# Kernel optimization log

Measured on AMD Instinct MI355X. Metric: run time of the kernel, lower is better.

## Reference

```python
import jax, jax.numpy as jnp
import numpy as np

DIM = 256
HEADS = 4
DIM_HEAD = 32
HIDDEN = HEADS * DIM_HEAD  # 128
SCALE = DIM_HEAD ** -0.5
EPS = 1e-5


def setup_inputs() -> dict:
    key = jax.random.key(0)
    ks = jax.random.split(key, 6)
    B, H, W = 32, 64, 64
    x = jax.random.normal(ks[0], (B, DIM, H, W), dtype=jnp.float32)
    w_qkv = jax.random.normal(ks[1], (3 * HIDDEN, DIM), dtype=jnp.float32) * (DIM ** -0.5)
    w_out = jax.random.normal(ks[2], (DIM, HIDDEN), dtype=jnp.float32) * (HIDDEN ** -0.5)
    b_out = jnp.zeros((DIM,), dtype=jnp.float32)
    g = jnp.ones((DIM,), dtype=jnp.float32)
    b = jnp.zeros((DIM,), dtype=jnp.float32)
    return {"x": x, "w_qkv": w_qkv, "w_out": w_out, "b_out": b_out, "g": g, "b": b}


def reference(x, w_qkv, w_out, b_out, g, b):
    B, C, H, W = x.shape
    n = H * W
    # 1x1 conv qkv projection (no bias)
    qkv = jnp.einsum('oc,bchw->bohw', w_qkv, x)  # [B, 3*HIDDEN, H, W]
    qkv = qkv.reshape(B, 3, HEADS, DIM_HEAD, n)  # [B, 3, h, d, n]
    q, k, v = qkv[:, 0], qkv[:, 1], qkv[:, 2]
    q = jax.nn.softmax(q, axis=-2) * SCALE       # softmax over head dim d
    k = jax.nn.softmax(k, axis=-1)               # softmax over tokens n
    context = jnp.einsum('bhdn,bhen->bhde', k, v)
    out = jnp.einsum('bhde,bhdn->bhen', context, q)  # [B, h, e, n]
    out = out.reshape(B, HIDDEN, H, W)
    # 1x1 conv output projection with bias
    out = jnp.einsum('oc,bchw->bohw', w_out, out) + b_out[None, :, None, None]
    # LayerNorm over channel dim (biased variance)
    mean = jnp.mean(out, axis=1, keepdims=True)
    var = jnp.var(out, axis=1, keepdims=True)
    out = (out - mean) / jnp.sqrt(var + EPS) * g[None, :, None, None] + b[None, :, None, None]
    return out
```

## Files before the change

### kernel.cpp

```cpp
#include <hip/hip_runtime.h>
#include <math.h>

#define NPIX 4096
#define BATCH 32
#define CDIM 256
#define SCALE_F 0.17677669529663687f
#define EPS_F 1e-5f

typedef _Float16 f16;
typedef _Float16 f16x8 __attribute__((ext_vector_type(8)));
typedef _Float16 f16x4 __attribute__((ext_vector_type(4)));
typedef float    f32x4 __attribute__((ext_vector_type(4)));

static __device__ __forceinline__ f32x4 mfma16(f16x8 a, f16x8 b, f32x4 c) {
    return __builtin_amdgcn_mfma_f32_16x16x32_f16(a, b, c, 0, 0, 0);
}

__global__ __launch_bounds__(256)
void wconv(const float* __restrict__ w, f16* __restrict__ wh)
{
    int i = blockIdx.x * 256 + threadIdx.x;
    float4 v = ((const float4*)w)[i];
    f16x4 o = {(f16)v.x, (f16)v.y, (f16)v.z, (f16)v.w};
    ((f16x4*)wh)[i] = o;
}

__global__ __launch_bounds__(256)
void qkv_fused(const f16* __restrict__ wh, const float* __restrict__ x,
               f16* __restrict__ qhatT, float* __restrict__ ctx,
               float* __restrict__ ksum)
{
    __shared__ __align__(16) f16 As[384 * 32];
    __shared__ __align__(16) f16 Bs[64 * 32];
    __shared__ __align__(16) f16 ek_s[128 * 64];
    __shared__ __align__(16) f16 v_s[128 * 64];

    const int b = blockIdx.y;
    const int t = threadIdx.x;
    const int lane = t & 63, w = t >> 6;
    const int lane15 = lane & 15, lg = lane >> 4;
    const int grow = w * 96;

    const float* xb = x + (size_t)b * 256 * NPIX;
    f16* qT = qhatT + (size_t)b * NPIX * 128;

    const int bn = t & 63;
    const int bc = t >> 6;
    const int bsw = bn * 32 + ((bc ^ ((bn >> 1) & 3)) << 3);

    f32x4 ctxacc[2][2];
    const f32x4 z4 = {0.f, 0.f, 0.f, 0.f};
    ctxacc[0][0] = z4; ctxacc[0][1] = z4; ctxacc[1][0] = z4; ctxacc[1][1] = z4;

    for (int tile = 0; tile < 4; tile++) {
        const int n0 = blockIdx.x * 256 + tile * 64;
        f32x4 acc[6][4];
        #pragma unroll
        for (int i = 0; i < 6; i++)
            #pragma unroll
            for (int j = 0; j < 4; j++) acc[i][j] = z4;

        float v8[8];
        #pragma unroll
        for (int m = 0; m < 8; m++)
            v8[m] = xb[(size_t)(bc * 8 + m) * NPIX + n0 + bn];

        for (int ks = 0; ks < 8; ks++) {
            const int k0 = ks * 32;
            #pragma unroll
            for (int it = 0; it < 6; it++) {
                int c = t + it * 256;
                int row = c >> 2, ch = c & 3;
                *(f16x8*)&As[row * 32 + ((ch ^ ((row >> 1) & 3)) << 3)] =
                    *(const f16x8*)&wh[(size_t)row * 256 + k0 + ch * 8];
            }
            f16x8 bv;
            #pragma unroll
            for (int m = 0; m < 8; m++) bv[m] = (f16)v8[m];
            *(f16x8*)&Bs[bsw] = bv;
            __syncthreads();
            if (ks < 7) {
                #pragma unroll
                for (int m = 0; m < 8; m++)
                    v8[m] = xb[(size_t)(k0 + 32 + bc * 8 + m) * NPIX + n0 + bn];
            }
            f16x8 bf[4];
            #pragma unroll
            for (int j = 0; j < 4; j++) {
                int rr = j * 16 + lane15;
                bf[j] = *(const f16x8*)&Bs[rr * 32 + ((lg ^ ((rr >> 1) & 3)) << 3)];
            }
            #pragma unroll
            for (int i = 0; i < 6; i++) {
                int rr = grow + i * 16 + lane15;
                f16x8 af = *(const f16x8*)&As[rr * 32 + ((lg ^ ((rr >> 1) & 3)) << 3)];
                #pragma unroll
                for (int j = 0; j < 4; j++)
                    acc[i][j] = mfma16(af, bf[j], acc[i][j]);
            }
            __syncthreads();
        }

        #pragma unroll
        for (int i = 0; i < 6; i++) {
            const int rbase = grow + i * 16;
            if (rbase < 128) {
                if ((rbase & 31) == 0) {
                    #pragma unroll
                    for (int j = 0; j < 4; j++) {
                        float e0[2][4]; float s = 0.f;
                        #pragma unroll
                        for (int ii = 0; ii < 2; ii++)
                            #pragma unroll
                            for (int r = 0; r < 4; r++) {
                                float ev = __expf(acc[i + ii][j][r]);
                                e0[ii][r] = ev; s += ev;
                            }
                        s += __shfl_xor(s, 16); s += __shfl_xor(s, 32);
                        float inv = SCALE_F / s;
                        int n = n0 + j * 16 + lane15;
                        #pragma unroll
                        for (int ii = 0; ii < 2; ii++) {
                            int d0 = rbase + ii * 16 + lg * 4;
                            f16x4 pk;
                            #pragma unroll
                            for (int r = 0; r < 4; r++) pk[r] = (f16)(e0[ii][r] * inv);
                            *(f16x4*)(qT + (size_t)n * 128 + d0) = pk;
                        }
                    }
                }
            } else if (rbase < 256) {
                const int kb = rbase - 128;
                #pragma unroll
                for (int r = 0; r < 4; r++) {
                    int row = kb + lg * 4 + r;
                    float p = 0.f;
                    #pragma unroll
                    for (int j = 0; j < 4; j++) {
                        float ev = __expf(acc[i][j][r]);
                        p += ev;
                        int col = j * 16 + lane15;
                        ek_s[row * 64 + ((((col >> 3) ^ (row & 7)) << 3) | (col & 7))] =
                            (f16)ev;
                    }
                    p += __shfl_xor(p, 1); p += __shfl_xor(p, 2);
                    p += __shfl_xor(p, 4); p += __shfl_xor(p, 8);
                    if (lane15 == 0) atomicAdd(&ksum[b * 128 + row], p);
                }
            } else {
                const int vb = rbase - 256;
                #pragma unroll
                for (int r = 0; r < 4; r++) {
                    int row = vb + lg * 4 + r;
                    #pragma unroll
                    for (int j = 0; j < 4; j++) {
                        int col = j * 16 + lane15;
                        v_s[row * 64 + ((((col >> 3) ^ (row & 7)) << 3) | (col & 7))] =
                            (f16)acc[i][j][r];
                    }
                }
            }
        }
        __syncthreads();
        #pragma unroll
        for (int ks2 = 0; ks2 < 2; ks2++) {
            f16x8 a2[2], b2[2];
            #pragma unroll
            for (int i2 = 0; i2 < 2; i2++) {
                int row = w * 32 + i2 * 16 + lane15;
                int off = row * 64 + (((ks2 * 4 + lg) ^ (row & 7)) << 3);
                a2[i2] = *(const f16x8*)&ek_s[off];
                b2[i2] = *(const f16x8*)&v_s[off];
            }
            #pragma unroll
            for (int i2 = 0; i2 < 2; i2++)
                #pragma unroll
                for (int j2 = 0; j2 < 2; j2++)
                    ctxacc[i2][j2] = mfma16(a2[i2], b2[j2], ctxacc[i2][j2]);
        }
    }

    float* cg = ctx + ((size_t)b * 4 + w) * 1024;
    #pragma unroll
    for (int i2 = 0; i2 < 2; i2++)
        #pragma unroll
        for (int j2 = 0; j2 < 2; j2++)
            #pragma unroll
            for (int r = 0; r < 4; r++)
                atomicAdd(&cg[(i2 * 16 + lg * 4 + r) * 32 + j2 * 16 + lane15],
                          ctxacc[i2][j2][r]);
}

__global__ __launch_bounds__(256)
void weff_kernel(const float* __restrict__ wout, const float* __restrict__ ctx,
                 const float* __restrict__ ksum, f16* __restrict__ weff)
{
    const int bh = blockIdx.x;
    const int b = bh >> 2, h = bh & 3;
    __shared__ float cs[1024];
    __shared__ float inv_s[32];
    const int t = threadIdx.x;
    for (int i = t; i < 1024; i += 256) cs[i] = ctx[(size_t)bh * 1024 + i];
    if (t < 32) inv_s[t] = 1.f / ksum[b * 128 + h * 32 + t];
    __syncthreads();
    float acc[32] = {};
    const float* wrow = wout + (size_t)t * 128 + h * 32;
    for (int e = 0; e < 32; e++) {
        float wv = wrow[e];
        #pragma unroll
        for (int d = 0; d < 32; d++) acc[d] += wv * cs[d * 32 + e];
    }
    f16* wo = weff + ((size_t)b * 256 + t) * 128 + h * 32;
    #pragma unroll
    for (int d = 0; d < 32; d++) wo[d] = (f16)(acc[d] * inv_s[d]);
}

__global__ __launch_bounds__(256)
void out_mfma_ln(const f16* __restrict__ weff, const f16* __restrict__ qhatT,
                 const float* __restrict__ bias, const float* __restrict__ g,
                 const float* __restrict__ bb, float* __restrict__ out)
{
    __shared__ __align__(16) f16 As2[256 * 32];
    __shared__ __align__(16) f16 Bs2[128 * 32];
    __shared__ float pb[256], pg[256], pbb[256];
    __shared__ float lds_s[4][128], lds_s2[4][128];
    const int b = blockIdx.y;
    const int tileN = blockIdx.x * 128;
    const int t = threadIdx.x;
    const int lane = t & 63, w = t >> 6;
    const int lane15 = lane & 15, lg = lane >> 4;
    pb[t] = bias[t]; pg[t] = g[t]; pbb[t] = bb[t];
    const f16* Aw = weff + (size_t)b * 256 * 128;
    const f16* Bw = qhatT + (size_t)b * NPIX * 128;
    f32x4 acc[4][8];
    const f32x4 z4 = {0.f, 0.f, 0.f, 0.f};
    #pragma unroll
    for (int i = 0; i < 4; i++)
        #pragma unroll
        for (int j = 0; j < 8; j++) acc[i][j] = z4;

    for (int k0 = 0; k0 < 128; k0 += 32) {
        #pragma unroll
        for (int it = 0; it < 4; it++) {
            int c = t + it * 256;
            int row = c >> 2, koff = (c & 3) * 8;
            *(f16x8*)&As2[row * 32 + koff] = *(const f16x8*)&Aw[(size_t)row * 128 + k0 + koff];
        }
        #pragma unroll
        for (int it = 0; it < 2; it++) {
            int c = t + it * 256;
            int row = c >> 2, koff = (c & 3) * 8;
            *(f16x8*)&Bs2[row * 32 + koff] =
                *(const f16x8*)&Bw[(size_t)(tileN + row) * 128 + k0 + koff];
        }
        __syncthreads();
        f16x8 af[4], bf[8];
        #pragma unroll
        for (int i = 0; i < 4; i++)
            af[i] = *(const f16x8*)&As2[(w * 64 + i * 16 + lane15) * 32 + lg * 8];
        #pragma unroll
        for (int j = 0; j < 8; j++)
            bf[j] = *(const f16x8*)&Bs2[(j * 16 + lane15) * 32 + lg * 8];
        #pragma unroll
        for (int i = 0; i < 4; i++)
            #pragma unroll
            for (int j = 0; j < 8; j++)
                acc[i][j] = mfma16(af[i], bf[j], acc[i][j]);
        __syncthreads();
    }
    #pragma unroll
    for (int i = 0; i < 4; i++)
        #pragma unroll
        for (int r = 0; r < 4; r++) {
            float bo = pb[w * 64 + i * 16 + lg * 4 + r];
            #pragma unroll
            for (int j = 0; j < 8; j++) acc[i][j][r] += bo;
        }
    #pragma unroll
    for (int j = 0; j < 8; j++) {
        float s = 0.f, s2 = 0.f;
        #pragma unroll
        for (int i = 0; i < 4; i++)
            #pragma unroll
            for (int r = 0; r < 4; r++) { float v = acc[i][j][r]; s += v; s2 += v * v; }
        s += __shfl_xor(s, 16);  s += __shfl_xor(s, 32);
        s2 += __shfl_xor(s2, 16); s2 += __shfl_xor(s2, 32);
        if (lg == 0) { lds_s[w][j * 16 + lane15] = s; lds_s2[w][j * 16 + lane15] = s2; }
    }
    __syncthreads();
    float mean[8], rstd[8];
    #pragma unroll
    for (int j = 0; j < 8; j++) {
        int col = j * 16 + lane15;
        float S = lds_s[0][col] + lds_s[1][col] + lds_s[2][col] + lds_s[3][col];
        float S2 = lds_s2[0][col] + lds_s2[1][col] + lds_s2[2][col] + lds_s2[3][col];
        float mn = S * (1.f / 256.f);
        mean[j] = mn;
        rstd[j] = rsqrtf(S2 * (1.f / 256.f) - mn * mn + EPS_F);
    }
    float* ob = out + (size_t)b * CDIM * NPIX;
    #pragma unroll
    for (int i = 0; i < 4; i++)
        #pragma unroll
        for (int r = 0; r < 4; r++) {
            int row = w * 64 + i * 16 + lg * 4 + r;
            float gm = pg[row], bt = pbb[row];
            #pragma unroll
            for (int j = 0; j < 8; j++)
                ob[(size_t)row * NPIX + tileN + j * 16 + lane15] =
                    (acc[i][j][r] - mean[j]) * rstd[j] * gm + bt;
        }
}

extern "C" void kernel_launch(void* const* d_in, const int* in_sizes, int n_in,
                              void* d_out, int out_size, void* d_ws, size_t ws_size,
                              hipStream_t stream)
{
    const float* x     = (const float*)d_in[0];
    const float* w_qkv = (const float*)d_in[1];
    const float* w_out = (const float*)d_in[2];
    const float* b_out = (const float*)d_in[3];
    const float* g     = (const float*)d_in[4];
    const float* bvec  = (const float*)d_in[5];
    float* out = (float*)d_out;

    char* wsb = (char*)d_ws;
    f16*   qhatT = (f16*)wsb;
    float* ctx   = (float*)(wsb + 33554432);
    float* ksum  = (float*)(wsb + 34078720);
    f16*   weff  = (f16*)(wsb + 34095104);
    f16*   wh    = (f16*)(wsb + 36192256);

    hipMemsetAsync(ctx, 0, 540672, stream);
    wconv<<<96, 256, 0, stream>>>(w_qkv, wh);
    qkv_fused<<<dim3(16, BATCH), 256, 0, stream>>>(wh, x, qhatT, ctx, ksum);
    weff_kernel<<<128, 256, 0, stream>>>(w_out, ctx, ksum, weff);
    out_mfma_ln<<<dim3(32, BATCH), 256, 0, stream>>>(weff, qhatT, b_out, g, bvec, out);
}
```

Baseline: 349.3 us.

## Load QKV weight fragments directly from global into registers with double-buffered B tile

Removes the shared-memory staging of the 384x32 weight tile. Each lane now loads its MFMA A fragments straight from global (L2-resident) memory into registers, and they are prefetched one k-step ahead. The x tile uses two shared buffers, which cuts one barrier per k-step and overlaps the next loads with the MFMAs. This frees LDS and barrier overhead, at the cost of more VGPRs and uncoalesced global loads of the weights.

Result: slower. 416.6 us (+19.3%).

```diff
diff --git a/kernel.cpp b/kernel.cpp
--- a/kernel.cpp
+++ b/kernel.cpp
@@ -30,8 +30,7 @@
                f16* __restrict__ qhatT, float* __restrict__ ctx,
                float* __restrict__ ksum)
 {
-    __shared__ __align__(16) f16 As[384 * 32];
-    __shared__ __align__(16) f16 Bs[64 * 32];
+    __shared__ __align__(16) f16 Bs[2][64 * 32];
     __shared__ __align__(16) f16 ek_s[128 * 64];
     __shared__ __align__(16) f16 v_s[128 * 64];
 
@@ -48,10 +47,23 @@
     const int bc = t >> 6;
     const int bsw = bn * 32 + ((bc ^ ((bn >> 1) & 3)) << 3);
 
+    const f16* Ab = wh + (size_t)(grow + lane15) * 256 + lg * 8;
+
     f32x4 ctxacc[2][2];
     const f32x4 z4 = {0.f, 0.f, 0.f, 0.f};
     ctxacc[0][0] = z4; ctxacc[0][1] = z4; ctxacc[1][0] = z4; ctxacc[1][1] = z4;
 
+    f16x8 af[6], af2[6];
+    float v8[8];
+    {
+        const int n00 = blockIdx.x * 256;
+        #pragma unroll
+        for (int i = 0; i < 6; i++) af[i] = *(const f16x8*)&Ab[i * 4096];
+        #pragma unroll
+        for (int m2 = 0; m2 < 8; m2++)
+            v8[m2] = xb[(size_t)(bc * 8 + m2) * NPIX + n00 + bn];
+    }
+
     for (int tile = 0; tile < 4; tile++) {
         const int n0 = blockIdx.x * 256 + tile * 64;
         f32x4 acc[6][4];
@@ -60,45 +72,75 @@
             #pragma unroll
             for (int j = 0; j < 4; j++) acc[i][j] = z4;
 
-        float v8[8];
-        #pragma unroll
-        for (int m = 0; m < 8; m++)
-            v8[m] = xb[(size_t)(bc * 8 + m) * NPIX + n0 + bn];
-
-        for (int ks = 0; ks < 8; ks++) {
-            const int k0 = ks * 32;
-            #pragma unroll
-            for (int it = 0; it < 6; it++) {
-                int c = t + it * 256;
-                int row = c >> 2, ch = c & 3;
-                *(f16x8*)&As[row * 32 + ((ch ^ ((row >> 1) & 3)) << 3)] =
-                    *(const f16x8*)&wh[(size_t)row * 256 + k0 + ch * 8];
-            }
-            f16x8 bv;
-            #pragma unroll
-            for (int m = 0; m < 8; m++) bv[m] = (f16)v8[m];
-            *(f16x8*)&Bs[bsw] = bv;
+        #pragma unroll
+        for (int m = 0; m < 4; m++) {
+            {
+                f16x8 bv;
+                #pragma unroll
+                for (int m2 = 0; m2 < 8; m2++) bv[m2] = (f16)v8[m2];
+                *(f16x8*)&Bs[0][bsw] = bv;
+            }
             __syncthreads();
-            if (ks < 7) {
-                #pragma unroll
-                for (int m = 0; m < 8; m++)
-                    v8[m] = xb[(size_t)(k0 + 32 + bc * 8 + m) * NPIX + n0 + bn];
-            }
-            f16x8 bf[4];
-            #pragma unroll
-            for (int j = 0; j < 4; j++) {
-                int rr = j * 16 + lane15;
-                bf[j] = *(const f16x8*)&Bs[rr * 32 + ((lg ^ ((rr >> 1) & 3)) << 3)];
-            }
-            #pragma unroll
-            for (int i = 0; i < 6; i++) {
-                int rr = grow + i * 16 + lane15;
-                f16x8 af = *(const f16x8*)&As[rr * 32 + ((lg ^ ((rr >> 1) & 3)) << 3)];
-                #pragma unroll
-                for (int j = 0; j < 4; j++)
-                    acc[i][j] = mfma16(af, bf[j], acc[i][j]);
+            {
+                const int k1 = m * 64 + 32;
+                #pragma unroll
+                for (int i = 0; i < 6; i++)
+                    af2[i] = *(const f16x8*)&Ab[i * 4096 + k1];
+                #pragma unroll
+                for (int m2 = 0; m2 < 8; m2++)
+                    v8[m2] = xb[(size_t)(k1 + bc * 8 + m2) * NPIX + n0 + bn];
+            }
+            {
+                f16x8 bf[4];
+                #pragma unroll
+                for (int j = 0; j < 4; j++) {
+                    int rr = j * 16 + lane15;
+                    bf[j] = *(const f16x8*)&Bs[0][rr * 32 + ((lg ^ ((rr >> 1) & 3)) << 3)];
+                }
+                #pragma unroll
+                for (int i = 0; i < 6; i++)
+                    #pragma unroll
+                    for (int j = 0; j < 4; j++)
+                        acc[i][j] = mfma16(af[i], bf[j], acc[i][j]);
+            }
+            {
+                f16x8 bv;
+                #pragma unroll
+                for (int m2 = 0; m2 < 8; m2++) bv[m2] = (f16)v8[m2];
+                *(f16x8*)&Bs[1][bsw] = bv;
             }
             __syncthreads();
+            if (m < 3) {
+                const int k2 = m * 64 + 64;
+                #pragma unroll
+                for (int i = 0; i < 6; i++)
+                    af[i] = *(const f16x8*)&Ab[i * 4096 + k2];
+                #pragma unroll
+                for (int m2 = 0; m2 < 8; m2++)
+                    v8[m2] = xb[(size_t)(k2 + bc * 8 + m2) * NPIX + n0 + bn];
+            }
+            {
+                f16x8 bf[4];
+                #pragma unroll
+                for (int j = 0; j < 4; j++) {
+                    int rr = j * 16 + lane15;
+                    bf[j] = *(const f16x8*)&Bs[1][rr * 32 + ((lg ^ ((rr >> 1) & 3)) << 3)];
+                }
+                #pragma unroll
+                for (int i = 0; i < 6; i++)
+                    #pragma unroll
+                    for (int j = 0; j < 4; j++)
+                        acc[i][j] = mfma16(af2[i], bf[j], acc[i][j]);
+            }
+        }
+
+        if (tile < 3) {
+            const int n1 = n0 + 64;
+            #pragma unroll
+            for (int i = 0; i < 6; i++) af[i] = *(const f16x8*)&Ab[i * 4096];
+            #pragma unroll
+            for (int m2 = 0; m2 < 8; m2++)
+                v8[m2] = xb[(size_t)(bc * 8 + m2) * NPIX + n1 + bn];
         }
 
         #pragma unroll
```

## Stage full x tile in LDS, read weights directly from global, localize ksum atomics

Applied to the files above, without the earlier changes.

The QKV GEMM now loads the whole 64x256 x tile into shared memory once per tile and reads weight fragments straight from global/L2 into registers, so the per-k-step __syncthreads and the shared-memory staging of weights go away. The k-loop now runs without barriers. Key-sum partials are accumulated in a shared array and flushed with one global atomic per row per block, which cuts global atomic traffic. The trade-off is more global weight reads per wave and the loss of the old prefetch overlap of x loads with MFMA.

Result: slower. 417.6 us (+19.6%).

```diff
diff --git a/kernel.cpp b/kernel.cpp
--- a/kernel.cpp
+++ b/kernel.cpp
@@ -30,10 +30,10 @@
                f16* __restrict__ qhatT, float* __restrict__ ctx,
                float* __restrict__ ksum)
 {
-    __shared__ __align__(16) f16 As[384 * 32];
-    __shared__ __align__(16) f16 Bs[64 * 32];
+    __shared__ __align__(16) f16 xt_s[64 * 256];
     __shared__ __align__(16) f16 ek_s[128 * 64];
     __shared__ __align__(16) f16 v_s[128 * 64];
+    __shared__ float ksum_s[128];
 
     const int b = blockIdx.y;
     const int t = threadIdx.x;
@@ -43,62 +43,55 @@
 
     const float* xb = x + (size_t)b * 256 * NPIX;
     f16* qT = qhatT + (size_t)b * NPIX * 128;
-
-    const int bn = t & 63;
-    const int bc = t >> 6;
-    const int bsw = bn * 32 + ((bc ^ ((bn >> 1) & 3)) << 3);
+    const f16* Ab = wh + (size_t)(grow + lane15) * 256 + lg * 8;
+
+    if (t < 128) ksum_s[t] = 0.f;
 
     f32x4 ctxacc[2][2];
     const f32x4 z4 = {0.f, 0.f, 0.f, 0.f};
     ctxacc[0][0] = z4; ctxacc[0][1] = z4; ctxacc[1][0] = z4; ctxacc[1][1] = z4;
 
+    #pragma unroll 1
     for (int tile = 0; tile < 4; tile++) {
         const int n0 = blockIdx.x * 256 + tile * 64;
+
+        #pragma unroll 2
+        for (int g = 0; g < 8; g++) {
+            float v8[8];
+            #pragma unroll
+            for (int m = 0; m < 8; m++)
+                v8[m] = xb[(size_t)(w * 64 + g * 8 + m) * NPIX + n0 + lane];
+            f16x8 bv;
+            #pragma unroll
+            for (int m = 0; m < 8; m++) bv[m] = (f16)v8[m];
+            const int c5 = w * 8 + g;
+            *(f16x8*)&xt_s[lane * 256 + ((c5 ^ (lane & 7)) << 3)] = bv;
+        }
+        __syncthreads();
+
         f32x4 acc[6][4];
         #pragma unroll
         for (int i = 0; i < 6; i++)
             #pragma unroll
             for (int j = 0; j < 4; j++) acc[i][j] = z4;
 
-        float v8[8];
-        #pragma unroll
-        for (int m = 0; m < 8; m++)
-            v8[m] = xb[(size_t)(bc * 8 + m) * NPIX + n0 + bn];
-
+        #pragma unroll 1
         for (int ks = 0; ks < 8; ks++) {
-            const int k0 = ks * 32;
-            #pragma unroll
-            for (int it = 0; it < 6; it++) {
-                int c = t + it * 256;
-                int row = c >> 2, ch = c & 3;
-                *(f16x8*)&As[row * 32 + ((ch ^ ((row >> 1) & 3)) << 3)] =
-                    *(const f16x8*)&wh[(size_t)row * 256 + k0 + ch * 8];
+            f16x8 af[6], bf[4];
+            #pragma unroll
+            for (int i = 0; i < 6; i++)
+                af[i] = *(const f16x8*)&Ab[(size_t)i * 4096 + ks * 32];
+            #pragma unroll
+            for (int j = 0; j < 4; j++) {
+                const int px = j * 16 + lane15;
+                bf[j] = *(const f16x8*)&xt_s[px * 256 +
+                                             (((ks * 4 + lg) ^ (px & 7)) << 3)];
             }
-            f16x8 bv;
-            #pragma unroll
-            for (int m = 0; m < 8; m++) bv[m] = (f16)v8[m];
-            *(f16x8*)&Bs[bsw] = bv;
-            __syncthreads();
-            if (ks < 7) {
-                #pragma unroll
-                for (int m = 0; m < 8; m++)
-                    v8[m] = xb[(size_t)(k0 + 32 + bc * 8 + m) * NPIX + n0 + bn];
-            }
-            f16x8 bf[4];
-            #pragma unroll
-            for (int j = 0; j < 4; j++) {
-                int rr = j * 16 + lane15;
-                bf[j] = *(const f16x8*)&Bs[rr * 32 + ((lg ^ ((rr >> 1) & 3)) << 3)];
-            }
-            #pragma unroll
-            for (int i = 0; i < 6; i++) {
-                int rr = grow + i * 16 + lane15;
-                f16x8 af = *(const f16x8*)&As[rr * 32 + ((lg ^ ((rr >> 1) & 3)) << 3)];
+            #pragma unroll
+            for (int i = 0; i < 6; i++)
                 #pragma unroll
                 for (int j = 0; j < 4; j++)
-                    acc[i][j] = mfma16(af, bf[j], acc[i][j]);
-            }
-            __syncthreads();
+                    acc[i][j] = mfma16(af[i], bf[j], acc[i][j]);
         }
 
         #pragma unroll
@@ -145,7 +138,7 @@
                     }
                     p += __shfl_xor(p, 1); p += __shfl_xor(p, 2);
                     p += __shfl_xor(p, 4); p += __shfl_xor(p, 8);
-                    if (lane15 == 0) atomicAdd(&ksum[b * 128 + row], p);
+                    if (lane15 == 0) atomicAdd(&ksum_s[row], p);
                 }
             } else {
                 const int vb = rbase - 256;
@@ -180,6 +173,8 @@
         }
     }
 
+    if (t < 128) atomicAdd(&ksum[b * 128 + t], ksum_s[t]);
+
     float* cg = ctx + ((size_t)b * 4 + w) * 1024;
     #pragma unroll
     for (int i2 = 0; i2 < 2; i2++)
```
